# Optimization experiments

Measured on AMD Instinct MI355X. Metric: run time of the kernel, lower is better.

Reference implementation:

```python
import jax, jax.numpy as jnp
import numpy as np
from jax import lax

B, K, C, P = 16, 4096, 256, 1024
NSAMPLE = 16
RADIUS = 0.3
NUM_CLASS, NUMD = 18, 1
OUT_CH = 3 + NUMD + NUM_CLASS  # 22
EPS = 1e-5


def fps(xyz, npoint):
    # furthest point sampling; xyz (B,N,3) -> (B,npoint) int32
    b, n, _ = xyz.shape
    def body(carry, _):
        mind, last = carry
        lx = jnp.take_along_axis(xyz, last[:, None, None], axis=1)  # (B,1,3)
        d = jnp.sum((xyz - lx) ** 2, -1)
        mind = jnp.minimum(mind, d)
        nxt = jnp.argmax(mind, -1).astype(jnp.int32)
        return (mind, nxt), nxt
    i0 = jnp.zeros((b,), jnp.int32)
    _, rest = lax.scan(body, (jnp.full((b, n), 1e10, xyz.dtype), i0), None, length=npoint - 1)
    return jnp.concatenate([i0[None], rest], 0).T  # (B,npoint)


def ball_query(xyz, new_xyz, radius, nsample):
    # first `nsample` points (in index order) within radius; pad with first hit
    k = xyz.shape[1]
    d2 = jnp.sum((new_xyz[:, :, None, :] - xyz[:, None, :, :]) ** 2, -1)  # (B,P,K)
    keyi = jnp.where(d2 < radius * radius, jnp.arange(k, dtype=jnp.int32), k)
    idx = jnp.sort(keyi, axis=-1)[..., :nsample]  # (B,P,S)
    first = idx[..., :1]
    idx = jnp.where(idx >= k, first, idx)
    return jnp.clip(idx, 0, k - 1)


def bn(x, g, b, axes):
    # BatchNorm (training-mode batch statistics), channel on last axis
    m = jnp.mean(x, axes, keepdims=True)
    v = jnp.var(x, axes, keepdims=True)
    return (x - m) * lax.rsqrt(v + EPS) * g + b


def setup_inputs() -> dict:
    key = jax.random.key(0)
    ks = jax.random.split(key, 24)
    s = 0.02
    inp = {
        'xyz': jax.random.normal(ks[0], (B, K, 3), jnp.float32),
        'features': jax.random.normal(ks[1], (B, C, K), jnp.float32),
        # shared MLP (Conv2d 1x1, no bias, followed by BN2d)
        'mlp_w0': jax.random.normal(ks[2], (128, C + 3), jnp.float32) * s,
        'mlp_g0': jnp.ones((128,), jnp.float32), 'mlp_be0': jnp.zeros((128,), jnp.float32),
        'mlp_w1': jax.random.normal(ks[3], (128, 128), jnp.float32) * s,
        'mlp_g1': jnp.ones((128,), jnp.float32), 'mlp_be1': jnp.zeros((128,), jnp.float32),
        'mlp_w2': jax.random.normal(ks[4], (128, 128), jnp.float32) * s,
        'mlp_g2': jnp.ones((128,), jnp.float32), 'mlp_be2': jnp.zeros((128,), jnp.float32),
        # head: conv1d(128,128)+bn, conv1d(128,128)+bn, conv1d(128,22)
        'w1': jax.random.normal(ks[5], (128, 128), jnp.float32) * s, 'b1': jnp.zeros((128,), jnp.float32),
        'g1': jnp.ones((128,), jnp.float32), 'be1': jnp.zeros((128,), jnp.float32),
        'w2': jax.random.normal(ks[6], (128, 128), jnp.float32) * s, 'b2': jnp.zeros((128,), jnp.float32),
        'g2': jnp.ones((128,), jnp.float32), 'be2': jnp.zeros((128,), jnp.float32),
        'w3': jax.random.normal(ks[7], (OUT_CH, 128), jnp.float32) * s, 'b3': jnp.zeros((OUT_CH,), jnp.float32),
    }
    return inp


def reference(xyz, features, mlp_w0, mlp_g0, mlp_be0, mlp_w1, mlp_g1, mlp_be1,
              mlp_w2, mlp_g2, mlp_be2, w1, b1, g1, be1, w2, b2, g2, be2, w3, b3):
    # --- vote aggregation: FPS + ball query + grouped shared-MLP + max pool ---
    fps_idx = fps(xyz, P)                                   # (B,P)
    new_xyz = jax.vmap(lambda p, i: p[i])(xyz, fps_idx)      # (B,P,3)
    gidx = ball_query(lax.stop_gradient(xyz), lax.stop_gradient(new_xyz), RADIUS, NSAMPLE)
    gxyz = jax.vmap(lambda p, i: p[i])(xyz, gidx)            # (B,P,S,3)
    gxyz = (gxyz - new_xyz[:, :, None, :]) / RADIUS          # normalize_xyz
    feats_t = jnp.swapaxes(features, 1, 2)                   # (B,K,C)
    gfeat = jax.vmap(lambda f, i: f[i])(feats_t, gidx)       # (B,P,S,C)
    h = jnp.concatenate([gxyz, gfeat], -1)                   # (B,P,S,3+C) use_xyz
    for w, g, b in ((mlp_w0, mlp_g0, mlp_be0), (mlp_w1, mlp_g1, mlp_be1), (mlp_w2, mlp_g2, mlp_be2)):
        h = jax.nn.relu(bn(jnp.einsum('bpsc,oc->bpso', h, w), g, b, (0, 1, 2)))
    agg = jnp.max(h, axis=2)                                 # (B,P,128)
    # --- conv1d + BN + ReLU head ---
    n1 = jax.nn.relu(bn(jnp.einsum('bpc,oc->bpo', agg, w1) + b1, g1, be1, (0, 1)))
    n2 = jax.nn.relu(bn(jnp.einsum('bpc,oc->bpo', n1, w2) + b2, g2, be2, (0, 1)))
    net = jnp.einsum('bpc,oc->bpo', n2, w3) + b3             # (B,P,3+numd+num_class)
    # --- decode_scores (mode='') ---
    center = new_xyz + net[..., :3]
    return jnp.concatenate([center, net[..., 3:]], -1)        # (B,P,22)
```

## Files before the change

kernel.cpp:

```cpp
#include <hip/hip_runtime.h>
#include <math.h>

#define Bsz 16
#define Kpt 4096
#define Cft 256
#define Pnp 1024
#define Smp 16
#define OUTCH 22
#define M0 (Bsz * Pnp * Smp)
#define M1 (Bsz * Pnp)

#define OFF_FT      ((size_t)0)
#define OFF_YA      ((size_t)8388608)
#define OFF_M2      ((size_t)25165824)
#define OFF_AGG     ((size_t)27262976)
#define OFF_YF1     ((size_t)28311552)
#define OFF_YF2     ((size_t)29360128)
#define OFF_W0T     ((size_t)31457280)
#define OFF_W1T     ((size_t)31473664)
#define OFF_W2T     ((size_t)31481856)
#define OFF_WF1T    ((size_t)31490048)
#define OFF_WF2T    ((size_t)31498240)
#define OFF_STATS   ((size_t)31506432)
#define OFF_GIDX    ((size_t)31507712)
#define OFF_NEWXYZ  ((size_t)31769856)

typedef __attribute__((ext_vector_type(8))) short bf16x8;
typedef __attribute__((ext_vector_type(4))) float f32x4;

__device__ __forceinline__ unsigned short f2bf(float x) {
    union { float f; unsigned u; } v; v.f = x;
    unsigned r = v.u + 0x7fffu + ((v.u >> 16) & 1u);
    return (unsigned short)(r >> 16);
}
__device__ __forceinline__ float bf2f(unsigned short u) {
    union { unsigned u; float f; } v; v.u = ((unsigned)u) << 16; return v.f;
}

template <int CTRL>
__device__ __forceinline__ unsigned long long dpp_max_step(unsigned long long key) {
    int lo = (int)(unsigned)key, hi = (int)(key >> 32);
    int slo = __builtin_amdgcn_update_dpp(0, lo, CTRL, 0xf, 0xf, true);
    int shi = __builtin_amdgcn_update_dpp(0, hi, CTRL, 0xf, 0xf, true);
    unsigned long long other = ((unsigned long long)(unsigned)shi << 32) | (unsigned)slo;
    return other > key ? other : key;
}

__global__ __launch_bounds__(256) void fps_fused(const float* __restrict__ xyz, float* __restrict__ new_xyz,
                                                 const float* __restrict__ features, unsigned short* __restrict__ ft,
                                                 const float* __restrict__ w0, const float* __restrict__ w1m,
                                                 const float* __restrict__ w2m, const float* __restrict__ wf1,
                                                 const float* __restrict__ wf2,
                                                 unsigned short* __restrict__ W0T, unsigned short* __restrict__ W1T,
                                                 unsigned short* __restrict__ W2T, unsigned short* __restrict__ WF1T,
                                                 unsigned short* __restrict__ WF2T) {
    __shared__ float4 xyz_s[Kpt];
    __shared__ unsigned long long red[2][4];
    int bid = blockIdx.x, tid = threadIdx.x;

    if (bid < 16) {
        int b = bid, wid = tid >> 6, lane = tid & 63;
        for (int k = tid; k < Kpt; k += 256) {
            float x = xyz[(size_t)b * Kpt * 3 + k * 3 + 0];
            float y = xyz[(size_t)b * Kpt * 3 + k * 3 + 1];
            float z = xyz[(size_t)b * Kpt * 3 + k * 3 + 2];
            xyz_s[k] = make_float4(x, y, z, 0.f);
        }
        __syncthreads();
        float px[16], py[16], pz[16], mind[16];
#pragma unroll
        for (int j = 0; j < 16; ++j) {
            float4 p = xyz_s[tid + j * 256];
            px[j] = p.x; py[j] = p.y; pz[j] = p.z;
            mind[j] = 1e10f;
        }
        float lx = xyz_s[0].x, ly = xyz_s[0].y, lz = xyz_s[0].z;
        if (tid == 0) {
            new_xyz[(size_t)b * Pnp * 3 + 0] = lx;
            new_xyz[(size_t)b * Pnp * 3 + 1] = ly;
            new_xyz[(size_t)b * Pnp * 3 + 2] = lz;
        }
        for (int it = 1; it < Pnp; ++it) {
            float bestv = -1.0f;
            int bestk = 0;
#pragma unroll
            for (int j = 0; j < 16; ++j) {
                float dx = __fsub_rn(px[j], lx);
                float dy = __fsub_rn(py[j], ly);
                float dz = __fsub_rn(pz[j], lz);
                float d = __fadd_rn(__fadd_rn(__fmul_rn(dx, dx), __fmul_rn(dy, dy)), __fmul_rn(dz, dz));
                float m = fminf(mind[j], d);
                mind[j] = m;
                if (m > bestv) { bestv = m; bestk = tid + j * 256; }
            }
            unsigned long long key = ((unsigned long long)__float_as_uint(bestv) << 32) | (unsigned)(~bestk);
            key = dpp_max_step<0x111>(key);
            key = dpp_max_step<0x112>(key);
            key = dpp_max_step<0x114>(key);
            key = dpp_max_step<0x118>(key);
            key = dpp_max_step<0x142>(key);
            key = dpp_max_step<0x143>(key);
            if (lane == 63) red[it & 1][wid] = key;
            __syncthreads();
            unsigned long long gkey = red[it & 1][0];
#pragma unroll
            for (int w = 1; w < 4; ++w) {
                unsigned long long ok = red[it & 1][w];
                if (ok > gkey) gkey = ok;
            }
            int win = (int)(~(unsigned)gkey);
            float4 c = xyz_s[win];
            lx = c.x; ly = c.y; lz = c.z;
            if (tid == 0) {
                size_t bp = (size_t)b * Pnp + it;
                new_xyz[bp * 3 + 0] = c.x;
                new_xyz[bp * 3 + 1] = c.y;
                new_xyz[bp * 3 + 2] = c.z;
            }
        }
    } else if (bid < 16 + 1024) {
        float* tile = (float*)xyz_s;
        int tx = tid & 31, ty = tid >> 5;
        int t0 = (bid - 16) * 16;
        for (int tt = 0; tt < 16; ++tt) {
            int t = t0 + tt;
            int k0 = (t & 127) << 5;
            int c0 = ((t >> 7) & 7) << 5;
            int b2 = t >> 10;
            __syncthreads();
#pragma unroll
            for (int j = 0; j < 4; ++j)
                tile[(ty + j * 8) * 33 + tx] = features[((size_t)b2 * Cft + c0 + ty + j * 8) * Kpt + k0 + tx];
            __syncthreads();
#pragma unroll
            for (int j = 0; j < 4; ++j)
                ft[((size_t)b2 * Kpt + k0 + ty + j * 8) * Cft + c0 + tx] = f2bf(tile[tx * 33 + ty + j * 8]);
        }
    } else {
        int base = (bid - (16 + 1024)) * 6144;
#pragma unroll 1
        for (int i = 0; i < 24; ++i) {
            int e = base + i * 256 + tid;
            const float* src; unsigned short* dst; int eo, stride, off;
            if (e < 32768) { src = w0; dst = W0T; eo = e; stride = 259; off = 3; }
            else {
                int r = e - 32768; int which = r >> 14; eo = r & 16383; stride = 128; off = 0;
                src = (which == 0) ? w1m : (which == 1) ? w2m : (which == 2) ? wf1 : wf2;
                dst = (which == 0) ? W1T : (which == 1) ? W2T : (which == 2) ? WF1T : WF2T;
            }
            int j = eo & 7, np = (eo >> 3) & 15, q = (eo >> 7) & 3, S = (eo >> 9) & 7, c = eo >> 12;
            dst[eo] = f2bf(src[(size_t)(S * 16 + np) * stride + off + c * 32 + q * 8 + j]);
        }
    }
}

__global__ __launch_bounds__(256) void ballq_kernel(const float* __restrict__ xyz, const float* __restrict__ new_xyz,
                                                    int* __restrict__ gidx) {
    __shared__ float xyz_s[Kpt * 3];
    __shared__ int idxbuf[64][16];
    __shared__ int have_s[64];
    int bx = blockIdx.x;
    int b = bx >> 4, chunk = bx & 15;
    int tid = threadIdx.x, w = tid >> 6, lane = tid & 63;
    for (int e = tid; e < Kpt * 3; e += 256) xyz_s[e] = xyz[(size_t)b * Kpt * 3 + e];
    __syncthreads();
    const float R2 = (float)(0.3 * 0.3);
    unsigned long long lmask = (lane == 63) ? 0x7fffffffffffffffull : ((1ull << lane) - 1ull);
    for (int t = 0; t < 16; ++t) {
        int ql = w * 16 + t;
        size_t bp = (size_t)b * Pnp + chunk * 64 + ql;
        float nx = new_xyz[bp * 3 + 0], ny = new_xyz[bp * 3 + 1], nz = new_xyz[bp * 3 + 2];
        int have = 0;
        for (int r = 0; r < 64; ++r) {
            int k = r * 64 + lane;
            float dx = __fsub_rn(nx, xyz_s[k * 3 + 0]);
            float dy = __fsub_rn(ny, xyz_s[k * 3 + 1]);
            float dz = __fsub_rn(nz, xyz_s[k * 3 + 2]);
            float d2 = __fadd_rn(__fadd_rn(__fmul_rn(dx, dx), __fmul_rn(dy, dy)), __fmul_rn(dz, dz));
            bool inb = d2 < R2;
            unsigned long long mask = __ballot(inb);
            if (mask) {
                int rank = __popcll(mask & lmask);
                if (inb && (have + rank) < 16) idxbuf[ql][have + rank] = k;
                have += __popcll(mask);
                if (have >= 16) break;
            }
        }
        if (lane == 0) have_s[ql] = (have > 16) ? 16 : have;
    }
    __syncthreads();
    for (int e = tid; e < 1024; e += 256) {
        int ql = e >> 4, slot = e & 15;
        int h = have_s[ql];
        int v = (h == 0) ? (Kpt - 1) : ((slot < h) ? idxbuf[ql][slot] : idxbuf[ql][0]);
        size_t bp = (size_t)b * Pnp + chunk * 64 + ql;
        gidx[bp * 16 + slot] = v;
    }
}

__global__ __launch_bounds__(256) void gemm0_mfma(const unsigned short* __restrict__ ft, const unsigned short* __restrict__ Bsw,
                                                  const float* __restrict__ xyz, const float* __restrict__ new_xyz,
                                                  const int* __restrict__ gidx, const float* __restrict__ w0,
                                                  unsigned short* __restrict__ yout, float* __restrict__ statsOut) {
    __shared__ unsigned short Asw[128 * 256];
    __shared__ unsigned short Bs[256 * 128];
    __shared__ float4 gxyz_s[128];
    __shared__ float4 w03s[128];
    __shared__ int krow_s[128];
    __shared__ float ssum[128], ssq[128];
    int tid = threadIdx.x;
    int wave = tid >> 6, lane = tid & 63, q = lane >> 4, l = lane & 15;
    int wm = wave >> 1, wn = wave & 1;
    size_t r0 = (size_t)blockIdx.x * 128;
    int b = (int)(r0 >> 14);

    if (tid < 128) {
        ssum[tid] = 0.f; ssq[tid] = 0.f;
        size_t r = r0 + tid;
        int kg = gidx[r];
        krow_s[tid] = kg;
        size_t bp = r >> 4;
        float gx = (xyz[((size_t)b * Kpt + kg) * 3 + 0] - new_xyz[bp * 3 + 0]) / 0.3f;
        float gy = (xyz[((size_t)b * Kpt + kg) * 3 + 1] - new_xyz[bp * 3 + 1]) / 0.3f;
        float gz = (xyz[((size_t)b * Kpt + kg) * 3 + 2] - new_xyz[bp * 3 + 2]) / 0.3f;
        gxyz_s[tid] = make_float4(gx, gy, gz, 0.f);
    } else {
        int o = tid - 128;
        w03s[o] = make_float4(w0[(size_t)o * 259 + 0], w0[(size_t)o * 259 + 1], w0[(size_t)o * 259 + 2], 0.f);
    }
#pragma unroll
    for (int i = 0; i < 16; ++i) {
        int e = i * 256 + tid;
        *(int4*)&Bs[e * 8] = *(const int4*)&Bsw[e * 8];
    }
    __syncthreads();
#pragma unroll
    for (int i = 0; i < 16; ++i) {
        int idx = i * 4 + wave;
        int G = idx >> 3, c = idx & 7;
        int kg = krow_s[G * 16 + l];
        const unsigned short* src = ft + ((size_t)b * Kpt + kg) * 256 + c * 32 + q * 8;
        *(int4*)&Asw[(size_t)((c * 8 + G) * 64 + lane) * 8] = *(const int4*)src;
    }
    __syncthreads();

    f32x4 acc[4][4];
    f32x4 zz = {0.f, 0.f, 0.f, 0.f};
#pragma unroll
    for (int mi = 0; mi < 4; ++mi)
#pragma unroll
        for (int ni = 0; ni < 4; ++ni) acc[mi][ni] = zz;

    for (int c = 0; c < 8; ++c) {
        bf16x8 af[4], bfr[4];
#pragma unroll
        for (int mi = 0; mi < 4; ++mi)
            af[mi] = *(const bf16x8*)&Asw[(size_t)((c * 8 + wm * 4 + mi) * 64 + lane) * 8];
#pragma unroll
        for (int ni = 0; ni < 4; ++ni)
            bfr[ni] = *(const bf16x8*)&Bs[(size_t)((c * 8 + wn * 4 + ni) * 64 + lane) * 8];
#pragma unroll
        for (int mi = 0; mi < 4; ++mi)
#pragma unroll
            for (int ni = 0; ni < 4; ++ni)
                acc[mi][ni] = __builtin_amdgcn_mfma_f32_16x16x32_bf16(af[mi], bfr[ni], acc[mi][ni], 0, 0, 0);
    }
    float4 wv[4];
#pragma unroll
    for (int ni = 0; ni < 4; ++ni) wv[ni] = w03s[wn * 64 + ni * 16 + l];
    float psum[4] = {0.f, 0.f, 0.f, 0.f}, psq[4] = {0.f, 0.f, 0.f, 0.f};
#pragma unroll
    for (int mi = 0; mi < 4; ++mi) {
#pragma unroll
        for (int r = 0; r < 4; ++r) {
            int mloc = wm * 64 + mi * 16 + q * 4 + r;
            float4 g = gxyz_s[mloc];
            size_t rowg = r0 + mloc;
#pragma unroll
            for (int ni = 0; ni < 4; ++ni) {
                int colg = wn * 64 + ni * 16 + l;
                float val = acc[mi][ni][r] + g.x * wv[ni].x + g.y * wv[ni].y + g.z * wv[ni].z;
                psum[ni] += val; psq[ni] += val * val;
                yout[rowg * 128 + colg] = f2bf(val);
            }
        }
    }
#pragma unroll
    for (int ni = 0; ni < 4; ++ni) {
        float s = psum[ni], sq = psq[ni];
        s += __shfl_xor(s, 16); sq += __shfl_xor(sq, 16);
        s += __shfl_xor(s, 32); sq += __shfl_xor(sq, 32);
        if (q == 0) {
            int colg = wn * 64 + ni * 16 + l;
            atomicAdd(&ssum[colg], s);
            atomicAdd(&ssq[colg], sq);
        }
    }
    __syncthreads();
    if (tid < 128) {
        atomicAdd(&statsOut[tid], ssum[tid]);
        atomicAdd(&statsOut[128 + tid], ssq[tid]);
    }
}

__global__ __launch_bounds__(256) void gemm_mfma_bn(const unsigned short* __restrict__ A, const unsigned short* __restrict__ Bsw,
                                                    unsigned short* __restrict__ OutBf, float* __restrict__ OutF,
                                                    const float* __restrict__ statsIn, const float* __restrict__ gamma,
                                                    const float* __restrict__ beta, const float* __restrict__ bias,
                                                    float invN, float* __restrict__ statsOut) {
    __shared__ unsigned short Asw[128 * 128];
    __shared__ unsigned short Bs[128 * 128];
    __shared__ float scs[128], shs[128], ssum[128], ssq[128];
    int tid = threadIdx.x;
    int wave = tid >> 6, lane = tid & 63, q = lane >> 4, l = lane & 15;
    int wm = wave >> 1, wn = wave & 1;
    size_t r0 = (size_t)blockIdx.x * 128;
    bool hasT = (statsIn != nullptr);
    if (tid < 128) {
        ssum[tid] = 0.f; ssq[tid] = 0.f;
        if (hasT) {
            float m = statsIn[tid] * invN;
            float v = statsIn[128 + tid] * invN - m * m;
            float sc = gamma[tid] / sqrtf(v + 1e-5f);
            scs[tid] = sc;
            shs[tid] = beta[tid] - m * sc;
        }
    }
#pragma unroll
    for (int i = 0; i < 8; ++i) {
        int e = i * 256 + tid;
        *(int4*)&Bs[e * 8] = *(const int4*)&Bsw[e * 8];
    }
    __syncthreads();
#pragma unroll
    for (int i = 0; i < 8; ++i) {
        int idx = i * 4 + wave;
        int G = idx >> 2, c = idx & 3;
        const unsigned short* src = A + (r0 + G * 16 + l) * 128 + c * 32 + q * 8;
        int4 v = *(const int4*)src;
        if (hasT) {
            unsigned short* u = (unsigned short*)&v;
            int cb = c * 32 + q * 8;
#pragma unroll
            for (int t = 0; t < 8; ++t) {
                float f = bf2f(u[t]);
                u[t] = f2bf(fmaxf(0.f, f * scs[cb + t] + shs[cb + t]));
            }
        }
        *(int4*)&Asw[(size_t)((c * 8 + G) * 64 + lane) * 8] = v;
    }
    __syncthreads();

    f32x4 acc[4][4];
    f32x4 zz = {0.f, 0.f, 0.f, 0.f};
#pragma unroll
    for (int mi = 0; mi < 4; ++mi)
#pragma unroll
        for (int ni = 0; ni < 4; ++ni) acc[mi][ni] = zz;

#pragma unroll
    for (int c = 0; c < 4; ++c) {
        bf16x8 af[4], bfr[4];
#pragma unroll
        for (int mi = 0; mi < 4; ++mi)
            af[mi] = *(const bf16x8*)&Asw[(size_t)((c * 8 + wm * 4 + mi) * 64 + lane) * 8];
#pragma unroll
        for (int ni = 0; ni < 4; ++ni)
            bfr[ni] = *(const bf16x8*)&Bs[(size_t)((c * 8 + wn * 4 + ni) * 64 + lane) * 8];
#pragma unroll
        for (int mi = 0; mi < 4; ++mi)
#pragma unroll
            for (int ni = 0; ni < 4; ++ni)
                acc[mi][ni] = __builtin_amdgcn_mfma_f32_16x16x32_bf16(af[mi], bfr[ni], acc[mi][ni], 0, 0, 0);
    }
    float psum[4] = {0.f, 0.f, 0.f, 0.f}, psq[4] = {0.f, 0.f, 0.f, 0.f};
#pragma unroll
    for (int mi = 0; mi < 4; ++mi) {
#pragma unroll
        for (int r = 0; r < 4; ++r) {
            size_t rowg = r0 + wm * 64 + mi * 16 + q * 4 + r;
#pragma unroll
            for (int ni = 0; ni < 4; ++ni) {
                int colg = wn * 64 + ni * 16 + l;
                float val = acc[mi][ni][r] + (bias ? bias[colg] : 0.f);
                psum[ni] += val; psq[ni] += val * val;
                if (OutBf) OutBf[rowg * 128 + colg] = f2bf(val);
                else OutF[rowg * 128 + colg] = val;
            }
        }
    }
#pragma unroll
    for (int ni = 0; ni < 4; ++ni) {
        float s = psum[ni], sq = psq[ni];
        s += __shfl_xor(s, 16); sq += __shfl_xor(sq, 16);
        s += __shfl_xor(s, 32); sq += __shfl_xor(sq, 32);
        if (q == 0) {
            int colg = wn * 64 + ni * 16 + l;
            atomicAdd(&ssum[colg], s);
            atomicAdd(&ssq[colg], sq);
        }
    }
    __syncthreads();
    if (tid < 128) {
        atomicAdd(&statsOut[tid], ssum[tid]);
        atomicAdd(&statsOut[128 + tid], ssq[tid]);
    }
}

__global__ __launch_bounds__(256) void gemm2_max(const unsigned short* __restrict__ A, const unsigned short* __restrict__ Bsw,
                                                 const float* __restrict__ statsIn, const float* __restrict__ gamma,
                                                 const float* __restrict__ beta, float invN,
                                                 float* __restrict__ m2, float* __restrict__ statsOut) {
    __shared__ unsigned short Asw[128 * 128];
    __shared__ unsigned short Bs[128 * 128];
    __shared__ float scs[128], shs[128], ssum[128], ssq[128];
    __shared__ float smax[8][128];
    int tid = threadIdx.x;
    int wave = tid >> 6, lane = tid & 63, q = lane >> 4, l = lane & 15;
    int wm = wave >> 1, wn = wave & 1;
    size_t r0 = (size_t)blockIdx.x * 128;
    if (tid < 128) {
        ssum[tid] = 0.f; ssq[tid] = 0.f;
        float m = statsIn[tid] * invN;
        float v = statsIn[128 + tid] * invN - m * m;
        float sc = gamma[tid] / sqrtf(v + 1e-5f);
        scs[tid] = sc;
        shs[tid] = beta[tid] - m * sc;
    }
#pragma unroll
    for (int i = 0; i < 8; ++i) {
        int e = i * 256 + tid;
        *(int4*)&Bs[e * 8] = *(const int4*)&Bsw[e * 8];
    }
    __syncthreads();
#pragma unroll
    for (int i = 0; i < 8; ++i) {
        int idx = i * 4 + wave;
        int G = idx >> 2, c = idx & 3;
        const unsigned short* src = A + (r0 + G * 16 + l) * 128 + c * 32 + q * 8;
        int4 v = *(const int4*)src;
        unsigned short* u = (unsigned short*)&v;
        int cb = c * 32 + q * 8;
#pragma unroll
        for (int t = 0; t < 8; ++t) {
            float f = bf2f(u[t]);
            u[t] = f2bf(fmaxf(0.f, f * scs[cb + t] + shs[cb + t]));
        }
        *(int4*)&Asw[(size_t)((c * 8 + G) * 64 + lane) * 8] = v;
    }
    __syncthreads();

    f32x4 acc[4][4];
    f32x4 zz = {0.f, 0.f, 0.f, 0.f};
#pragma unroll
    for (int mi = 0; mi < 4; ++mi)
#pragma unroll
        for (int ni = 0; ni < 4; ++ni) acc[mi][ni] = zz;

#pragma unroll
    for (int c = 0; c < 4; ++c) {
        bf16x8 af[4], bfr[4];
#pragma unroll
        for (int mi = 0; mi < 4; ++mi)
            af[mi] = *(const bf16x8*)&Asw[(size_t)((c * 8 + wm * 4 + mi) * 64 + lane) * 8];
#pragma unroll
        for (int ni = 0; ni < 4; ++ni)
            bfr[ni] = *(const bf16x8*)&Bs[(size_t)((c * 8 + wn * 4 + ni) * 64 + lane) * 8];
#pragma unroll
        for (int mi = 0; mi < 4; ++mi)
#pragma unroll
            for (int ni = 0; ni < 4; ++ni)
                acc[mi][ni] = __builtin_amdgcn_mfma_f32_16x16x32_bf16(af[mi], bfr[ni], acc[mi][ni], 0, 0, 0);
    }
    float psum[4] = {0.f, 0.f, 0.f, 0.f}, psq[4] = {0.f, 0.f, 0.f, 0.f};
#pragma unroll
    for (int mi = 0; mi < 4; ++mi) {
#pragma unroll
        for (int ni = 0; ni < 4; ++ni) {
            float gm = -1e30f;
#pragma unroll
            for (int r = 0; r < 4; ++r) {
                float val = acc[mi][ni][r];
                psum[ni] += val; psq[ni] += val * val;
                gm = fmaxf(gm, val);
            }
            gm = fmaxf(gm, __shfl_xor(gm, 16));
            gm = fmaxf(gm, __shfl_xor(gm, 32));
            if (q == 0) smax[wm * 4 + mi][wn * 64 + ni * 16 + l] = gm;
        }
    }
#pragma unroll
    for (int ni = 0; ni < 4; ++ni) {
        float s = psum[ni], sq = psq[ni];
        s += __shfl_xor(s, 16); sq += __shfl_xor(sq, 16);
        s += __shfl_xor(s, 32); sq += __shfl_xor(sq, 32);
        if (q == 0) {
            int colg = wn * 64 + ni * 16 + l;
            atomicAdd(&ssum[colg], s);
            atomicAdd(&ssq[colg], sq);
        }
    }
    __syncthreads();
#pragma unroll
    for (int i = 0; i < 4; ++i) {
        int e = i * 256 + tid;
        int g = e >> 7, cc = e & 127;
        m2[((size_t)blockIdx.x * 8 + g) * 128 + cc] = smax[g][cc];
    }
    if (tid < 128) {
        atomicAdd(&statsOut[tid], ssum[tid]);
        atomicAdd(&statsOut[128 + tid], ssq[tid]);
    }
}

__global__ __launch_bounds__(256) void maxpool2(const float* __restrict__ m2, const float* __restrict__ st,
                                                const float* __restrict__ gamma, const float* __restrict__ beta,
                                                unsigned short* __restrict__ agg) {
    __shared__ float sc_s[128], sh_s[128];
    int tid = threadIdx.x;
    if (tid < 128) {
        const float invN = 1.f / (float)M0;
        float m = st[tid] * invN;
        float v = st[128 + tid] * invN - m * m;
        float sc = gamma[tid] / sqrtf(v + 1e-5f);
        sc_s[tid] = sc;
        sh_s[tid] = beta[tid] - m * sc;
    }
    __syncthreads();
    size_t base = (size_t)blockIdx.x * 1024;
#pragma unroll
    for (int j = 0; j < 4; ++j) {
        size_t idx = base + j * 256 + tid;
        int col = (int)(idx & 127);
        float v = m2[idx];
        agg[idx] = f2bf(fmaxf(0.f, v * sc_s[col] + sh_s[col]));
    }
}

__global__ __launch_bounds__(256) void final_k(const float* __restrict__ yf, const float* __restrict__ st,
                                               const float* __restrict__ gamma, const float* __restrict__ beta,
                                               const float* __restrict__ w3, const float* __restrict__ b3,
                                               const float* __restrict__ new_xyz, float* __restrict__ out) {
    __shared__ float n2s[8][128];
    __shared__ float w3s[22 * 132];
    __shared__ float scf[128], shf[128];
    int tid = threadIdx.x;
    size_t r0 = (size_t)blockIdx.x * 8;
    if (tid < 128) {
        const float invN = 1.f / (float)M1;
        float m = st[tid] * invN;
        float v = st[128 + tid] * invN - m * m;
        float sc = gamma[tid] / sqrtf(v + 1e-5f);
        scf[tid] = sc;
        shf[tid] = beta[tid] - m * sc;
    }
    __syncthreads();
#pragma unroll
    for (int i = 0; i < 4; ++i) {
        int e = tid + i * 256;
        int rl = e >> 7, c = e & 127;
        float raw = yf[(r0 + rl) * 128 + c];
        n2s[rl][c] = fmaxf(0.f, raw * scf[c] + shf[c]);
    }
#pragma unroll
    for (int i = 0; i < 11; ++i) {
        int e = tid + i * 256;
        int o = e >> 7, c = e & 127;
        w3s[o * 132 + c] = w3[e];
    }
    __syncthreads();
    int rl = tid >> 5, o = tid & 31;
    if (o < OUTCH) {
        float dot = 0.f;
#pragma unroll 4
        for (int c = 0; c < 128; ++c) dot += n2s[rl][c] * w3s[o * 132 + c];
        float v = dot + b3[o];
        if (o < 3) v += new_xyz[(r0 + rl) * 3 + o];
        out[(r0 + rl) * OUTCH + o] = v;
    }
}

extern "C" void kernel_launch(void* const* d_in, const int* in_sizes, int n_in,
                              void* d_out, int out_size, void* d_ws, size_t ws_size,
                              hipStream_t stream) {
    (void)in_sizes; (void)n_in; (void)out_size; (void)ws_size;
    const float* xyz = (const float*)d_in[0];
    const float* features = (const float*)d_in[1];
    const float* w0 = (const float*)d_in[2];
    const float* g0 = (const float*)d_in[3];
    const float* be0 = (const float*)d_in[4];
    const float* w1m = (const float*)d_in[5];
    const float* g1m = (const float*)d_in[6];
    const float* be1m = (const float*)d_in[7];
    const float* w2m = (const float*)d_in[8];
    const float* g2m = (const float*)d_in[9];
    const float* be2m = (const float*)d_in[10];
    const float* wf1 = (const float*)d_in[11];
    const float* bf1 = (const float*)d_in[12];
    const float* gf1 = (const float*)d_in[13];
    const float* bef1 = (const float*)d_in[14];
    const float* wf2 = (const float*)d_in[15];
    const float* bf2 = (const float*)d_in[16];
    const float* gf2 = (const float*)d_in[17];
    const float* bef2 = (const float*)d_in[18];
    const float* w3 = (const float*)d_in[19];
    const float* b3 = (const float*)d_in[20];
    float* ws = (float*)d_ws;
    unsigned short* ft = (unsigned short*)(ws + OFF_FT);
    unsigned short* yA = (unsigned short*)(ws + OFF_YA);
    float* m2 = ws + OFF_M2;
    unsigned short* agg = (unsigned short*)(ws + OFF_AGG);
    unsigned short* yF1 = (unsigned short*)(ws + OFF_YF1);
    float* yF2 = ws + OFF_YF2;
    unsigned short* W0T = (unsigned short*)(ws + OFF_W0T);
    unsigned short* W1T = (unsigned short*)(ws + OFF_W1T);
    unsigned short* W2T = (unsigned short*)(ws + OFF_W2T);
    unsigned short* WF1T = (unsigned short*)(ws + OFF_WF1T);
    unsigned short* WF2T = (unsigned short*)(ws + OFF_WF2T);
    float* st = ws + OFF_STATS;
    int* gidx = (int*)(ws + OFF_GIDX);
    float* nxyz = ws + OFF_NEWXYZ;

    hipMemsetAsync((void*)st, 0, 5 * 256 * sizeof(float), stream);

    fps_fused<<<16 + 1024 + 16, 256, 0, stream>>>(xyz, nxyz, features, ft,
                                                  w0, w1m, w2m, wf1, wf2,
                                                  W0T, W1T, W2T, WF1T, WF2T);
    ballq_kernel<<<256, 256, 0, stream>>>(xyz, nxyz, gidx);

    gemm0_mfma<<<M0 / 128, 256, 0, stream>>>(ft, W0T, xyz, nxyz, gidx, w0, yA, st);
    gemm_mfma_bn<<<M0 / 128, 256, 0, stream>>>(yA, W1T, yA, nullptr, st, g0, be0, nullptr,
                                               1.f / (float)M0, st + 256);
    gemm2_max<<<M0 / 128, 256, 0, stream>>>(yA, W2T, st + 256, g1m, be1m, 1.f / (float)M0,
                                            m2, st + 512);
    maxpool2<<<M1 * 128 / 1024, 256, 0, stream>>>(m2, st + 512, g2m, be2m, agg);

    gemm_mfma_bn<<<M1 / 128, 256, 0, stream>>>(agg, WF1T, yF1, nullptr, nullptr, nullptr, nullptr,
                                               bf1, 0.f, st + 768);
    gemm_mfma_bn<<<M1 / 128, 256, 0, stream>>>(yF1, WF2T, nullptr, yF2, st + 768, gf1, bef1,
                                               bf2, 1.f / (float)M1, st + 1024);
    final_k<<<M1 / 8, 256, 0, stream>>>(yF2, st + 1024, gf2, bef2, w3, b3, nxyz, (float*)d_out);
}
```

Baseline: 1.074 ms.

## Fuse maxpool BN into head GEMM load and shard BN stat atomics

Removes the separate maxpool2 kernel. The following head GEMM now reads the fp32 max-pooled values directly and applies BN+ReLU plus the bf16 conversion while loading A. BN statistic accumulation is split across 32 slots chosen by block index to reduce global atomic contention. Consumers sum the slots when computing scale and shift, which adds a few extra loads per block and a larger memset.

```diff
diff --git a/kernel.cpp b/kernel.cpp
--- a/kernel.cpp
+++ b/kernel.cpp
@@ -9,21 +9,23 @@
 #define OUTCH 22
 #define M0 (Bsz * Pnp * Smp)
 #define M1 (Bsz * Pnp)
+#define NSLOT 32
 
 #define OFF_FT      ((size_t)0)
 #define OFF_YA      ((size_t)8388608)
 #define OFF_M2      ((size_t)25165824)
-#define OFF_AGG     ((size_t)27262976)
-#define OFF_YF1     ((size_t)28311552)
-#define OFF_YF2     ((size_t)29360128)
-#define OFF_W0T     ((size_t)31457280)
-#define OFF_W1T     ((size_t)31473664)
-#define OFF_W2T     ((size_t)31481856)
-#define OFF_WF1T    ((size_t)31490048)
-#define OFF_WF2T    ((size_t)31498240)
-#define OFF_STATS   ((size_t)31506432)
-#define OFF_GIDX    ((size_t)31507712)
-#define OFF_NEWXYZ  ((size_t)31769856)
+#define OFF_YF1     ((size_t)27262976)
+#define OFF_YF2     ((size_t)28311552)
+#define OFF_W0T     ((size_t)30408704)
+#define OFF_W1T     ((size_t)30425088)
+#define OFF_W2T     ((size_t)30433280)
+#define OFF_WF1T    ((size_t)30441472)
+#define OFF_WF2T    ((size_t)30449664)
+#define OFF_STATS   ((size_t)30457856)
+#define OFF_GIDX    ((size_t)30498816)
+#define OFF_NEWXYZ  ((size_t)30760960)
+
+#define ST_STRIDE (NSLOT * 256)
 
 typedef __attribute__((ext_vector_type(8))) short bf16x8;
 typedef __attribute__((ext_vector_type(4))) float f32x4;
@@ -35,6 +37,15 @@
 }
 __device__ __forceinline__ float bf2f(unsigned short u) {
     union { unsigned u; float f; } v; v.u = ((unsigned)u) << 16; return v.f;
+}
+
+__device__ __forceinline__ void read_stats(const float* st, int tid, float& sm, float& sq) {
+    sm = 0.f; sq = 0.f;
+#pragma unroll
+    for (int s = 0; s < NSLOT; ++s) {
+        sm += st[s * 256 + tid];
+        sq += st[s * 256 + 128 + tid];
+    }
 }
 
 template <int CTRL>
@@ -298,12 +309,14 @@
     }
     __syncthreads();
     if (tid < 128) {
-        atomicAdd(&statsOut[tid], ssum[tid]);
-        atomicAdd(&statsOut[128 + tid], ssq[tid]);
-    }
-}
-
-__global__ __launch_bounds__(256) void gemm_mfma_bn(const unsigned short* __restrict__ A, const unsigned short* __restrict__ Bsw,
+        float* stSlot = statsOut + (blockIdx.x & (NSLOT - 1)) * 256;
+        atomicAdd(&stSlot[tid], ssum[tid]);
+        atomicAdd(&stSlot[128 + tid], ssq[tid]);
+    }
+}
+
+__global__ __launch_bounds__(256) void gemm_mfma_bn(const unsigned short* __restrict__ A, const float* __restrict__ Af32,
+                                                    const unsigned short* __restrict__ Bsw,
                                                     unsigned short* __restrict__ OutBf, float* __restrict__ OutF,
                                                     const float* __restrict__ statsIn, const float* __restrict__ gamma,
                                                     const float* __restrict__ beta, const float* __restrict__ bias,
@@ -319,8 +332,10 @@
     if (tid < 128) {
         ssum[tid] = 0.f; ssq[tid] = 0.f;
         if (hasT) {
-            float m = statsIn[tid] * invN;
-            float v = statsIn[128 + tid] * invN - m * m;
+            float sm, sq;
+            read_stats(statsIn, tid, sm, sq);
+            float m = sm * invN;
+            float v = sq * invN - m * m;
             float sc = gamma[tid] / sqrtf(v + 1e-5f);
             scs[tid] = sc;
             shs[tid] = beta[tid] - m * sc;
@@ -336,15 +351,30 @@
     for (int i = 0; i < 8; ++i) {
         int idx = i * 4 + wave;
         int G = idx >> 2, c = idx & 3;
-        const unsigned short* src = A + (r0 + G * 16 + l) * 128 + c * 32 + q * 8;
-        int4 v = *(const int4*)src;
-        if (hasT) {
+        int cb = c * 32 + q * 8;
+        int4 v;
+        if (Af32) {
+            const float* srcf = Af32 + (r0 + G * 16 + l) * 128 + cb;
+            float4 v0 = *(const float4*)srcf;
+            float4 v1 = *(const float4*)(srcf + 4);
+            float vv[8] = {v0.x, v0.y, v0.z, v0.w, v1.x, v1.y, v1.z, v1.w};
             unsigned short* u = (unsigned short*)&v;
-            int cb = c * 32 + q * 8;
 #pragma unroll
             for (int t = 0; t < 8; ++t) {
-                float f = bf2f(u[t]);
-                u[t] = f2bf(fmaxf(0.f, f * scs[cb + t] + shs[cb + t]));
+                float f = vv[t];
+                if (hasT) f = fmaxf(0.f, f * scs[cb + t] + shs[cb + t]);
+                u[t] = f2bf(f);
+            }
+        } else {
+            const unsigned short* src = A + (r0 + G * 16 + l) * 128 + cb;
+            v = *(const int4*)src;
+            if (hasT) {
+                unsigned short* u = (unsigned short*)&v;
+#pragma unroll
+                for (int t = 0; t < 8; ++t) {
+                    float f = bf2f(u[t]);
+                    u[t] = f2bf(fmaxf(0.f, f * scs[cb + t] + shs[cb + t]));
+                }
             }
         }
         *(int4*)&Asw[(size_t)((c * 8 + G) * 64 + lane) * 8] = v;
@@ -402,8 +432,9 @@
     }
     __syncthreads();
     if (tid < 128) {
-        atomicAdd(&statsOut[tid], ssum[tid]);
-        atomicAdd(&statsOut[128 + tid], ssq[tid]);
+        float* stSlot = statsOut + (blockIdx.x & (NSLOT - 1)) * 256;
+        atomicAdd(&stSlot[tid], ssum[tid]);
+        atomicAdd(&stSlot[128 + tid], ssq[tid]);
     }
 }
 
@@ -421,8 +452,10 @@
     size_t r0 = (size_t)blockIdx.x * 128;
     if (tid < 128) {
         ssum[tid] = 0.f; ssq[tid] = 0.f;
-        float m = statsIn[tid] * invN;
-        float v = statsIn[128 + tid] * invN - m * m;
+        float sm, sq;
+        read_stats(statsIn, tid, sm, sq);
+        float m = sm * invN;
+        float v = sq * invN - m * m;
         float sc = gamma[tid] / sqrtf(v + 1e-5f);
         scs[tid] = sc;
         shs[tid] = beta[tid] - m * sc;
@@ -508,32 +541,9 @@
         m2[((size_t)blockIdx.x * 8 + g) * 128 + cc] = smax[g][cc];
     }
     if (tid < 128) {
-        atomicAdd(&statsOut[tid], ssum[tid]);
-        atomicAdd(&statsOut[128 + tid], ssq[tid]);
-    }
-}
-
-__global__ __launch_bounds__(256) void maxpool2(const float* __restrict__ m2, const float* __restrict__ st,
-                                                const float* __restrict__ gamma, const float* __restrict__ beta,
-                                                unsigned short* __restrict__ agg) {
-    __shared__ float sc_s[128], sh_s[128];
-    int tid = threadIdx.x;
-    if (tid < 128) {
-        const float invN = 1.f / (float)M0;
-        float m = st[tid] * invN;
-        float v = st[128 + tid] * invN - m * m;
-        float sc = gamma[tid] / sqrtf(v + 1e-5f);
-        sc_s[tid] = sc;
-        sh_s[tid] = beta[tid] - m * sc;
-    }
-    __syncthreads();
-    size_t base = (size_t)blockIdx.x * 1024;
-#pragma unroll
-    for (int j = 0; j < 4; ++j) {
-        size_t idx = base + j * 256 + tid;
-        int col = (int)(idx & 127);
-        float v = m2[idx];
-        agg[idx] = f2bf(fmaxf(0.f, v * sc_s[col] + sh_s[col]));
+        float* stSlot = statsOut + (blockIdx.x & (NSLOT - 1)) * 256;
+        atomicAdd(&stSlot[tid], ssum[tid]);
+        atomicAdd(&stSlot[128 + tid], ssq[tid]);
     }
 }
 
@@ -548,8 +558,10 @@
     size_t r0 = (size_t)blockIdx.x * 8;
     if (tid < 128) {
         const float invN = 1.f / (float)M1;
-        float m = st[tid] * invN;
-        float v = st[128 + tid] * invN - m * m;
+        float sm, sq;
+        read_stats(st, tid, sm, sq);
+        float m = sm * invN;
+        float v = sq * invN - m * m;
         float sc = gamma[tid] / sqrtf(v + 1e-5f);
         scf[tid] = sc;
         shf[tid] = beta[tid] - m * sc;
@@ -609,7 +621,6 @@
     unsigned short* ft = (unsigned short*)(ws + OFF_FT);
     unsigned short* yA = (unsigned short*)(ws + OFF_YA);
     float* m2 = ws + OFF_M2;
-    unsigned short* agg = (unsigned short*)(ws + OFF_AGG);
     unsigned short* yF1 = (unsigned short*)(ws + OFF_YF1);
     float* yF2 = ws + OFF_YF2;
     unsigned short* W0T = (unsigned short*)(ws + OFF_W0T);
@@ -621,7 +632,7 @@
     int* gidx = (int*)(ws + OFF_GIDX);
     float* nxyz = ws + OFF_NEWXYZ;
 
-    hipMemsetAsync((void*)st, 0, 5 * 256 * sizeof(float), stream);
+    hipMemsetAsync((void*)st, 0, 5 * ST_STRIDE * sizeof(float), stream);
 
     fps_fused<<<16 + 1024 + 16, 256, 0, stream>>>(xyz, nxyz, features, ft,
                                                   w0, w1m, w2m, wf1, wf2,
@@ -629,15 +640,13 @@
     ballq_kernel<<<256, 256, 0, stream>>>(xyz, nxyz, gidx);
 
     gemm0_mfma<<<M0 / 128, 256, 0, stream>>>(ft, W0T, xyz, nxyz, gidx, w0, yA, st);
-    gemm_mfma_bn<<<M0 / 128, 256, 0, stream>>>(yA, W1T, yA, nullptr, st, g0, be0, nullptr,
-                                               1.f / (float)M0, st + 256);
-    gemm2_max<<<M0 / 128, 256, 0, stream>>>(yA, W2T, st + 256, g1m, be1m, 1.f / (float)M0,
-                                            m2, st + 512);
-    maxpool2<<<M1 * 128 / 1024, 256, 0, stream>>>(m2, st + 512, g2m, be2m, agg);
-
-    gemm_mfma_bn<<<M1 / 128, 256, 0, stream>>>(agg, WF1T, yF1, nullptr, nullptr, nullptr, nullptr,
-                                               bf1, 0.f, st + 768);
-    gemm_mfma_bn<<<M1 / 128, 256, 0, stream>>>(yF1, WF2T, nullptr, yF2, st + 768, gf1, bef1,
-                                               bf2, 1.f / (float)M1, st + 1024);
-    final_k<<<M1 / 8, 256, 0, stream>>>(yF2, st + 1024, gf2, bef2, w3, b3, nxyz, (float*)d_out);
-}
+    gemm_mfma_bn<<<M0 / 128, 256, 0, stream>>>(yA, nullptr, W1T, yA, nullptr,
+                                               st, g0, be0, nullptr, 1.f / (float)M0, st + ST_STRIDE);
+    gemm2_max<<<M0 / 128, 256, 0, stream>>>(yA, W2T, st + ST_STRIDE, g1m, be1m, 1.f / (float)M0,
+                                            m2, st + 2 * ST_STRIDE);
+    gemm_mfma_bn<<<M1 / 128, 256, 0, stream>>>(nullptr, m2, WF1T, yF1, nullptr,
+                                               st + 2 * ST_STRIDE, g2m, be2m, bf1, 1.f / (float)M0, st + 3 * ST_STRIDE);
+    gemm_mfma_bn<<<M1 / 128, 256, 0, stream>>>(yF1, nullptr, WF2T, nullptr, yF2,
+                                               st + 3 * ST_STRIDE, gf1, bef1, bf2, 1.f / (float)M1, st + 4 * ST_STRIDE);
+    final_k<<<M1 / 8, 256, 0, stream>>>(yF2, st + 4 * ST_STRIDE, gf2, bef2, w3, b3, nxyz, (float*)d_out);
+}
```

After: 1.013 ms. 5.7% less time.
